# Kernel optimization log

Measured on AMD Instinct MI355X. Metric: run time of the kernel, lower is better.

The kernel has to match this reference:

```python
import jax, jax.numpy as jnp
import numpy as np

CUTOFF = 8.0  # SMEAMConfig.cutoff


def _natural_cubic_coeffs(t, y):
    """Natural cubic spline coefficients. t: [K] knots, y: [K, 1] values.
    Returns per-interval (a, b, c, d), each [K-1, 1]."""
    h = t[1:] - t[:-1]                              # [K-1]
    dy = (y[1:] - y[:-1]) / h[:, None]              # [K-1, 1]
    rhs = 6.0 * (dy[1:] - dy[:-1])                  # [K-2, 1]
    main = 2.0 * (h[:-1] + h[1:])
    A = jnp.diag(main) + jnp.diag(h[1:-1], 1) + jnp.diag(h[1:-1], -1)
    m_int = jnp.linalg.solve(A, rhs)                # interior second derivatives
    z = jnp.zeros((1, y.shape[1]), dtype=y.dtype)
    M = jnp.concatenate([z, m_int, z], axis=0)      # natural BC: M0 = M_{K-1} = 0
    a = y[:-1]
    b = dy - h[:, None] * (2.0 * M[:-1] + M[1:]) / 6.0
    c = M[:-1] / 2.0
    d = (M[1:] - M[:-1]) / (6.0 * h[:, None])
    return a, b, c, d


def _spline_eval(t, coeffs, x):
    """Evaluate spline at x: [T] -> [T, 1]. Edge intervals extrapolate."""
    a, b, c, d = coeffs
    idx = jnp.clip(jnp.searchsorted(t, x, side='right') - 1, 0, t.shape[0] - 2)
    s = (x - t[idx])[:, None]
    return a[idx] + s * (b[idx] + s * (c[idx] + s * d[idx]))


def setup_inputs() -> dict:
    key = jax.random.key(0)
    N, deg, K = 10000, 32, 7
    E = N * deg
    k1, k2, k3, k4 = jax.random.split(key, 4)
    # edge displacement vectors; scaled so bond lengths fall inside [0, cutoff]
    r = jax.random.normal(k1, (E, 3), dtype=jnp.float32) * 2.0
    f_coeffs = jax.random.uniform(k2, (K, 1), dtype=jnp.float32)
    g_coeffs = jax.random.uniform(k3, (K, 1), dtype=jnp.float32)
    src = jax.random.randint(k4, (E,), 0, N, dtype=jnp.int32)
    # fixed in-degree layout: edges with destination j are indices [j*deg, (j+1)*deg)
    dst = jnp.repeat(jnp.arange(N, dtype=jnp.int32), deg)
    return {"r": r, "f_coeffs": f_coeffs, "g_coeffs": g_coeffs,
            "src": src, "dst": dst, "deg": deg}


def reference(r, f_coeffs, g_coeffs, src, dst, deg):
    E = r.shape[0]
    K = f_coeffs.shape[0]
    knots_radial = jnp.linspace(0.0, CUTOFF, K, dtype=r.dtype)
    knots_angular = jnp.linspace(-1.0, 1.0, K, dtype=r.dtype)
    f_c = _natural_cubic_coeffs(knots_radial, f_coeffs)
    g_c = _natural_cubic_coeffs(knots_angular, g_coeffs)

    # line-graph (non-backtracking) triplets: e1 ends where e2 starts
    e2 = jnp.repeat(jnp.arange(E, dtype=jnp.int32), deg)                    # [T]
    e1 = (src[:, None] * deg + jnp.arange(deg, dtype=jnp.int32)).ravel()    # [T]
    valid = src[e1] != dst[e2]   # exclude backtracking e2 = reverse(e1)

    r1 = -r[e1]                  # [T, 3]
    r2 = r[e2]                   # [T, 3]
    l1 = jnp.linalg.norm(r1, axis=1)
    l2 = jnp.linalg.norm(r2, axis=1)
    bond_cosine = jnp.clip(jnp.sum(r1 * r2, axis=1) / (l1 * l2), -1.0, 1.0)

    m = (_spline_eval(knots_radial, f_c, l1)
         * _spline_eval(knots_radial, f_c, l2)
         * _spline_eval(knots_angular, g_c, bond_cosine))    # [T, 1]
    m = jnp.where(valid[:, None], m, jnp.zeros((), dtype=m.dtype))

    # scatter-sum triplet messages onto destination edges (line-graph nodes)
    ft = jax.ops.segment_sum(m, e2, num_segments=E)           # [E, 1]
    return ft
```

## Files before the change

kernel.cpp:

```cpp
#include <hip/hip_runtime.h>
#include <hip/hip_fp16.h>

#define DEG 32
#define K_KNOTS 7
#define NINT 6

typedef _Float16 half_t;
typedef _Float16 h2 __attribute__((ext_vector_type(2)));

union UF8 {
    uint2 u;
    struct { h2 xy; h2 zf; } h;
};

__device__ inline float fdot2(h2 a, h2 b, float c) {
#if __has_builtin(__builtin_amdgcn_fdot2)
    return __builtin_amdgcn_fdot2(a, b, c, false);
#else
    return (float)a.x * (float)b.x + (float)a.y * (float)b.y + c;
#endif
}

__device__ inline void spline_coeffs(const float* __restrict__ y, float h, float4* C) {
    float dy[NINT];
#pragma unroll
    for (int i = 0; i < NINT; ++i) dy[i] = (y[i + 1] - y[i]) / h;
    float rhs[5];
#pragma unroll
    for (int i = 0; i < 5; ++i) rhs[i] = 6.0f * (dy[i + 1] - dy[i]);
    float cp[5], dp[5];
    float denom = 4.0f * h;
    cp[0] = h / denom;
    dp[0] = rhs[0] / denom;
#pragma unroll
    for (int i = 1; i < 5; ++i) {
        denom = 4.0f * h - h * cp[i - 1];
        cp[i] = h / denom;
        dp[i] = (rhs[i] - h * dp[i - 1]) / denom;
    }
    float M[K_KNOTS];
    M[0] = 0.0f; M[6] = 0.0f;
    M[5] = dp[4];
#pragma unroll
    for (int i = 3; i >= 0; --i) M[i + 1] = dp[i] - cp[i] * M[i + 2];
#pragma unroll
    for (int i = 0; i < NINT; ++i) {
        C[i].x = y[i];
        C[i].y = dy[i] - h * (2.0f * M[i] + M[i + 1]) * (1.0f / 6.0f);
        C[i].z = M[i] * 0.5f;
        C[i].w = (M[i + 1] - M[i]) / (6.0f * h);
    }
}

__global__ __launch_bounds__(256) void edge_kernel(
    const float* __restrict__ r, const float* __restrict__ fc,
    uint2* __restrict__ uf, int E) {
    __shared__ float4 sF[NINT];
    if (threadIdx.x == 0) {
        float4 c[NINT];
        spline_coeffs(fc, 8.0f / 6.0f, c);
#pragma unroll
        for (int i = 0; i < NINT; ++i) sF[i] = c[i];
    }
    __syncthreads();
    int e = blockIdx.x * blockDim.x + threadIdx.x;
    if (e >= E) return;
    float x = r[3 * e + 0];
    float y = r[3 * e + 1];
    float z = r[3 * e + 2];
    float d = x * x + y * y + z * z;
    float rl = rsqrtf(d);
    float l = d * rl;
    float u = l * (6.0f / 8.0f);
    int idx = (int)u;
    idx = idx < 0 ? 0 : (idx > NINT - 1 ? NINT - 1 : idx);
    float s = l - (8.0f / 6.0f) * (float)idx;
    float4 c = sF[idx];
    float f = c.x + s * (c.y + s * (c.z + s * c.w));
    UF8 q;
    q.h.xy.x = (half_t)(x * rl);
    q.h.xy.y = (half_t)(y * rl);
    q.h.zf.x = (half_t)(z * rl);
    q.h.zf.y = (half_t)f;
    uf[e] = q.u;
}

__global__ __launch_bounds__(256) void triplet_kernel(
    const uint2* __restrict__ uf, const float* __restrict__ gc,
    const int* __restrict__ src, const int* __restrict__ dst,
    float* __restrict__ out, int E) {
    __shared__ float4 sG[NINT];
    if (threadIdx.x == 0) {
        float4 c[NINT];
        spline_coeffs(gc, 2.0f / 6.0f, c);
#pragma unroll
        for (int i = 0; i < NINT; ++i) sG[i] = c[i];
    }
    __syncthreads();

    int t = blockIdx.x * blockDim.x + threadIdx.x;
    int e = t >> 2;
    int q = t & 3;
    if (e >= E) return;

    int a = src[e];
    int de = dst[e];
    UF8 qe; qe.u = uf[e];
    uint2 neg = qe.u;
    neg.x ^= 0x80008000u;
    neg.y ^= 0x00008000u;
    h2 ne_xy = __builtin_bit_cast(h2, neg.x);
    h2 ne_zf = __builtin_bit_cast(h2, neg.y);
    h2 ne_z0; ne_z0.x = ne_zf.x; ne_z0.y = (half_t)0.0f;
    float fe = (float)qe.h.zf.y;

    const uint4* blk = (const uint4*)(uf + (size_t)a * DEG);
    const int4* sblk = (const int4*)(src + (size_t)a * DEG);
    uint4 rq[4];
    int4 sq[2];
#pragma unroll
    for (int it = 0; it < 4; ++it) rq[it] = blk[q * 4 + it];
#pragma unroll
    for (int it = 0; it < 2; ++it) sq[it] = sblk[q * 2 + it];

    float acc = 0.0f;
#pragma unroll
    for (int rr = 0; rr < 8; ++rr) {
        uint4 qq = rq[rr >> 1];
        unsigned w0 = (rr & 1) ? qq.z : qq.x;
        unsigned w1 = (rr & 1) ? qq.w : qq.y;
        int4 sv = sq[rr >> 2];
        int s2 = (rr & 3) == 0 ? sv.x : (rr & 3) == 1 ? sv.y
               : (rr & 3) == 2 ? sv.z : sv.w;
        h2 kxy = __builtin_bit_cast(h2, w0);
        h2 kzf = __builtin_bit_cast(h2, w1);
        float cosv = fdot2(kxy, ne_xy, fdot2(kzf, ne_z0, 0.0f));
        cosv = fminf(fmaxf(cosv, -1.0f), 1.0f);
        float u = (cosv + 1.0f) * 3.0f;
        int idx = (int)u;
        idx = idx > NINT - 1 ? NINT - 1 : idx;
        float s = cosv - (-1.0f + (2.0f / 6.0f) * (float)idx);
        float4 c = sG[idx];
        float g = c.x + s * (c.y + s * (c.z + s * c.w));
        float fk = (float)kzf.y;
        float term = (s2 != de) ? fk * g : 0.0f;
        acc += term;
    }

    acc += __shfl_xor(acc, 1, 64);
    acc += __shfl_xor(acc, 2, 64);
    if (q == 0) out[e] = fe * acc;
}

extern "C" void kernel_launch(void* const* d_in, const int* in_sizes, int n_in,
                              void* d_out, int out_size, void* d_ws, size_t ws_size,
                              hipStream_t stream) {
    const float* r   = (const float*)d_in[0];
    const float* fc  = (const float*)d_in[1];
    const float* gc  = (const float*)d_in[2];
    const int* src   = (const int*)d_in[3];
    const int* dst   = (const int*)d_in[4];
    float* out = (float*)d_out;
    int E = in_sizes[3];

    uint2* uf = (uint2*)d_ws;

    int threads = 256;
    int blocks1 = (E + threads - 1) / threads;
    edge_kernel<<<blocks1, threads, 0, stream>>>(r, fc, uf, E);

    long long T2 = (long long)E * 4;
    int blocks2 = (int)((T2 + threads - 1) / threads);
    triplet_kernel<<<blocks2, threads, 0, stream>>>(uf, gc, src, dst, out, E);
}
```

Measured before the change: 82.05 us.

## Reorder triplet work by source node via counting sort for gather locality

Builds a counting sort of edges by source node (histogram, single-block scan, atomic scatter) and has the triplet kernel process edges in that order. Edges sharing a source then read the same 32-edge neighbor block close together in time, which is meant to improve cache reuse of the gathered uf/src data. This adds three extra kernel launches, global atomics, and a serial single-block scan. The output writes become scattered.

```diff
diff --git a/kernel.cpp b/kernel.cpp
--- a/kernel.cpp
+++ b/kernel.cpp
@@ -54,7 +54,7 @@
 
 __global__ __launch_bounds__(256) void edge_kernel(
     const float* __restrict__ r, const float* __restrict__ fc,
-    uint2* __restrict__ uf, int E) {
+    uint2* __restrict__ uf, int* __restrict__ cnt, int E, int N) {
     __shared__ float4 sF[NINT];
     if (threadIdx.x == 0) {
         float4 c[NINT];
@@ -64,6 +64,7 @@
     }
     __syncthreads();
     int e = blockIdx.x * blockDim.x + threadIdx.x;
+    if (e < N) cnt[e] = 0;
     if (e >= E) return;
     float x = r[3 * e + 0];
     float y = r[3 * e + 1];
@@ -85,10 +86,50 @@
     uf[e] = q.u;
 }
 
+__global__ __launch_bounds__(256) void hist_kernel(
+    const int* __restrict__ src, int* __restrict__ cnt, int E) {
+    int e = blockIdx.x * blockDim.x + threadIdx.x;
+    if (e < E) atomicAdd(&cnt[src[e]], 1);
+}
+
+__global__ __launch_bounds__(1024) void scan_kernel(
+    const int* __restrict__ cnt, int* __restrict__ cur, int N) {
+    __shared__ int buf[2][1024];
+    int tid = threadIdx.x;
+    int chunk = (N + 1023) >> 10;
+    int lo = tid * chunk;
+    int hi = lo + chunk;
+    if (lo > N) lo = N;
+    if (hi > N) hi = N;
+    int s = 0;
+    for (int i = lo; i < hi; ++i) s += cnt[i];
+    buf[0][tid] = s;
+    __syncthreads();
+    int pi = 0;
+    for (int off = 1; off < 1024; off <<= 1) {
+        int v = buf[pi][tid];
+        if (tid >= off) v += buf[pi][tid - off];
+        buf[pi ^ 1][tid] = v;
+        pi ^= 1;
+        __syncthreads();
+    }
+    int base = buf[pi][tid] - s;
+    for (int i = lo; i < hi; ++i) { cur[i] = base; base += cnt[i]; }
+}
+
+__global__ __launch_bounds__(256) void scatter_kernel(
+    const int* __restrict__ src, int* __restrict__ cur,
+    int* __restrict__ order, int E) {
+    int e = blockIdx.x * blockDim.x + threadIdx.x;
+    if (e >= E) return;
+    int p = atomicAdd(&cur[src[e]], 1);
+    order[p] = e;
+}
+
 __global__ __launch_bounds__(256) void triplet_kernel(
     const uint2* __restrict__ uf, const float* __restrict__ gc,
     const int* __restrict__ src, const int* __restrict__ dst,
-    float* __restrict__ out, int E) {
+    const int* __restrict__ order, float* __restrict__ out, int E) {
     __shared__ float4 sG[NINT];
     if (threadIdx.x == 0) {
         float4 c[NINT];
@@ -99,9 +140,10 @@
     __syncthreads();
 
     int t = blockIdx.x * blockDim.x + threadIdx.x;
-    int e = t >> 2;
+    int g = t >> 2;
     int q = t & 3;
-    if (e >= E) return;
+    if (g >= E) return;
+    int e = order[g];
 
     int a = src[e];
     int de = dst[e];
@@ -141,9 +183,9 @@
         idx = idx > NINT - 1 ? NINT - 1 : idx;
         float s = cosv - (-1.0f + (2.0f / 6.0f) * (float)idx);
         float4 c = sG[idx];
-        float g = c.x + s * (c.y + s * (c.z + s * c.w));
+        float g2 = c.x + s * (c.y + s * (c.z + s * c.w));
         float fk = (float)kzf.y;
-        float term = (s2 != de) ? fk * g : 0.0f;
+        float term = (s2 != de) ? fk * g2 : 0.0f;
         acc += term;
     }
 
@@ -162,14 +204,23 @@
     const int* dst   = (const int*)d_in[4];
     float* out = (float*)d_out;
     int E = in_sizes[3];
-
-    uint2* uf = (uint2*)d_ws;
+    int N = E / DEG;
+
+    char* ws = (char*)d_ws;
+    uint2* uf  = (uint2*)ws;
+    int* cnt   = (int*)(ws + (size_t)E * 8);
+    int* cur   = (int*)(ws + (size_t)E * 8 + (size_t)N * 4);
+    int* order = (int*)(ws + (size_t)E * 8 + (size_t)N * 8);
 
     int threads = 256;
-    int blocks1 = (E + threads - 1) / threads;
-    edge_kernel<<<blocks1, threads, 0, stream>>>(r, fc, uf, E);
+    int blocksE = (E + threads - 1) / threads;
+
+    edge_kernel<<<blocksE, threads, 0, stream>>>(r, fc, uf, cnt, E, N);
+    hist_kernel<<<blocksE, threads, 0, stream>>>(src, cnt, E);
+    scan_kernel<<<1, 1024, 0, stream>>>(cnt, cur, N);
+    scatter_kernel<<<blocksE, threads, 0, stream>>>(src, cur, order, E);
 
     long long T2 = (long long)E * 4;
     int blocks2 = (int)((T2 + threads - 1) / threads);
-    triplet_kernel<<<blocks2, threads, 0, stream>>>(uf, gc, src, dst, out, E);
-}
+    triplet_kernel<<<blocks2, threads, 0, stream>>>(uf, gc, src, dst, order, out, E);
+}
```

Result: slower. 136.6 us (+66.5%).
